# Optimization experiments

Hardware: AMD Instinct MI355X
Metric: run time of the kernel (lower is better)

Reference implementation:

```python
import jax, jax.numpy as jnp
import numpy as np

HIDDEN = 50
INPUT = 4

def setup_inputs() -> dict:
    key = jax.random.key(0)
    ks = jax.random.split(key, 7)
    B, T = 4096, 512
    s_ih = 1.0 / np.sqrt(HIDDEN)
    return {
        "x": jax.random.normal(ks[0], (B, T, INPUT), dtype=jnp.float32),
        "W_ih": jax.random.uniform(ks[1], (4 * HIDDEN, INPUT), jnp.float32, -s_ih, s_ih),
        "W_hh": jax.random.uniform(ks[2], (4 * HIDDEN, HIDDEN), jnp.float32, -s_ih, s_ih),
        "b_ih": jax.random.uniform(ks[3], (4 * HIDDEN,), jnp.float32, -s_ih, s_ih),
        "b_hh": jax.random.uniform(ks[4], (4 * HIDDEN,), jnp.float32, -s_ih, s_ih),
        "W_fc": jax.random.uniform(ks[5], (1, HIDDEN), jnp.float32, -s_ih, s_ih),
        "b_fc": jax.random.uniform(ks[6], (1,), jnp.float32, -s_ih, s_ih),
    }

def reference(x, W_ih, W_hh, b_ih, b_hh, W_fc, b_fc):
    B = x.shape[0]
    b = b_ih + b_hh  # fold biases once
    # precompute input projection for all timesteps: [B,T,4H]
    x_proj = jnp.einsum('btd,gd->btg', x, W_ih) + b
    h0 = jnp.zeros((B, HIDDEN), x.dtype)
    c0 = jnp.zeros((B, HIDDEN), x.dtype)

    def step(carry, xp_t):
        h, c = carry
        gates = xp_t + h @ W_hh.T  # [B,4H]
        i, f, g, o = jnp.split(gates, 4, axis=-1)  # PyTorch gate order i,f,g,o
        i = jax.nn.sigmoid(i)
        f = jax.nn.sigmoid(f)
        g = jnp.tanh(g)
        o = jax.nn.sigmoid(o)
        c_new = f * c + i * g
        h_new = o * jnp.tanh(c_new)
        return (h_new, c_new), None

    (h_T, _), _ = jax.lax.scan(step, (h0, c0), jnp.swapaxes(x_proj, 0, 1))
    # fc applied to last timestep only (out[:, -1, :])
    return h_T @ W_fc.T + b_fc  # [B,1]
```

## Files before the change

kernel.cpp:

```cpp
#include <hip/hip_runtime.h>


#define HID  50
#define NROW 200
#define TT   512
#define NIN  4
#define BT   16
#define KD   72
#define NW   8

typedef float f32x4 __attribute__((ext_vector_type(4)));
typedef short s16x8 __attribute__((ext_vector_type(8)));

__device__ __forceinline__ unsigned short f2bf(float f) {
    unsigned u = __builtin_bit_cast(unsigned, f);
    return (unsigned short)((u + 0x7FFF + ((u >> 16) & 1)) >> 16);
}
__device__ __forceinline__ float fast_sigmoid(float v) {
    float e = __builtin_amdgcn_exp2f(v * -1.442695040888963f);
    return __builtin_amdgcn_rcpf(1.0f + e);
}
__device__ __forceinline__ float fast_tanh(float v) {
    float e = __builtin_amdgcn_exp2f(v * -2.885390081777927f);
    return 2.0f * __builtin_amdgcn_rcpf(1.0f + e) - 1.0f;
}

__device__ __forceinline__ float wval(const float* W_hh, const float* W_ih,
                                      int rowp, int k) {
    if (rowp >= NROW) return 0.0f;
    const int ur = rowp >> 2, g = rowp & 3;
    const int a = k >> 4, b = k & 15;
    if (b <= 12) { const int u = 4 * b + a;
                   return (u < HID) ? W_hh[(g * HID + ur) * HID + u] : 0.0f; }
    if (b == 13) return W_ih[(g * HID + ur) * NIN + a];
    return 0.0f;
}

__global__ __launch_bounds__(64 * NW, 2)
void lstm_mfma3(const float* __restrict__ x,
                const float* __restrict__ W_ih,
                const float* __restrict__ W_hh,
                const float* __restrict__ b_ih,
                const float* __restrict__ b_hh,
                const float* __restrict__ W_fc,
                const float* __restrict__ b_fc,
                float* __restrict__ out)
{
    __shared__ __align__(16) unsigned short buf[2][BT][KD];
    __shared__ float red[BT];

    const int tid = threadIdx.x;
    const int w   = tid >> 6;
    const int l   = tid & 63;
    const int lr  = l & 15;
    const int lg  = l >> 4;
    const int b0  = blockIdx.x * BT;

    for (int i = tid; i < 2 * BT * KD; i += 64 * NW)
        ((unsigned short*)buf)[i] = 0;
    if (tid < BT) red[tid] = 0.0f;

    const bool two = (w < 5);
    const int  T0  = two ? w : (w + 5);
    const int  T1  = w + 5;

    s16x8 af0[2], af1[2];
    f32x4 bias0, bias1 = {0.f, 0.f, 0.f, 0.f};
    float wfc0 = 0.0f, wfc1 = 0.0f;
    {
        const int rowp = 16 * T0 + lr;
#pragma unroll
        for (int kh = 0; kh < 2; ++kh) {
            s16x8 f;
#pragma unroll
            for (int j = 0; j < 8; ++j)
                f[j] = (short)f2bf(wval(W_hh, W_ih, rowp, 32 * kh + 8 * lg + j));
            af0[kh] = f;
        }
#pragma unroll
        for (int r = 0; r < 4; ++r) {
            const int rr = 16 * T0 + 4 * lg + r;
            bias0[r] = (rr < NROW) ? (b_ih[(rr & 3) * HID + (rr >> 2)] +
                                      b_hh[(rr & 3) * HID + (rr >> 2)]) : 0.0f;
        }
        const int u = 4 * T0 + lg;
        wfc0 = (u < HID) ? W_fc[u] : 0.0f;
    }
    if (two) {
        const int rowp = 16 * T1 + lr;
#pragma unroll
        for (int kh = 0; kh < 2; ++kh) {
            s16x8 f;
#pragma unroll
            for (int j = 0; j < 8; ++j)
                f[j] = (short)f2bf(wval(W_hh, W_ih, rowp, 32 * kh + 8 * lg + j));
            af1[kh] = f;
        }
#pragma unroll
        for (int r = 0; r < 4; ++r) {
            const int rr = 16 * T1 + 4 * lg + r;
            bias1[r] = (rr < NROW) ? (b_ih[(rr & 3) * HID + (rr >> 2)] +
                                      b_hh[(rr & 3) * HID + (rr >> 2)]) : 0.0f;
        }
        const int u = 4 * T1 + lg;
        wfc1 = (u < HID) ? W_fc[u] : 0.0f;
    }

    const float* xg = x + ((size_t)(b0 + lr) * TT) * NIN + lg;
    if (w == 7) buf[0][lr][16 * lg + 13] = f2bf(xg[0]);
    __syncthreads();

    float c0 = 0.f, h0 = 0.f, c1 = 0.f, h1 = 0.f;

    for (int t = 0; t < TT; ++t) {
        const int p = t & 1;

        float xv = 0.0f;
        const bool xload = (w == 7) && (t + 1 < TT);
        if (xload) xv = xg[(size_t)(t + 1) * NIN];

        const s16x8 bf0v = *(const s16x8*)&buf[p][lr][8 * lg];
        const s16x8 bf1v = *(const s16x8*)&buf[p][lr][32 + 8 * lg];

        f32x4 a0 = bias0;
        a0 = __builtin_amdgcn_mfma_f32_16x16x32_bf16(af0[0], bf0v, a0, 0, 0, 0);
        a0 = __builtin_amdgcn_mfma_f32_16x16x32_bf16(af0[1], bf1v, a0, 0, 0, 0);
        f32x4 a1;
        if (two) {
            a1 = bias1;
            a1 = __builtin_amdgcn_mfma_f32_16x16x32_bf16(af1[0], bf0v, a1, 0, 0, 0);
            a1 = __builtin_amdgcn_mfma_f32_16x16x32_bf16(af1[1], bf1v, a1, 0, 0, 0);
        }

        if (xload) buf[p ^ 1][lr][16 * lg + 13] = f2bf(xv);

        {
            const float gi = fast_sigmoid(a0[0]);
            const float gf = fast_sigmoid(a0[1]);
            const float gg = fast_tanh(a0[2]);
            const float go = fast_sigmoid(a0[3]);
            c0 = gf * c0 + gi * gg;
            h0 = go * fast_tanh(c0);
        }
        if (two) {
            const float gi = fast_sigmoid(a1[0]);
            const float gf = fast_sigmoid(a1[1]);
            const float gg = fast_tanh(a1[2]);
            const float go = fast_sigmoid(a1[3]);
            c1 = gf * c1 + gi * gg;
            h1 = go * fast_tanh(c1);
            unsigned pk;
            asm("v_cvt_pk_bf16_f32 %0, %1, %2" : "=v"(pk) : "v"(h0), "v"(h1));
            buf[p ^ 1][lr][16 * lg + T0] = (unsigned short)pk;
            buf[p ^ 1][lr][16 * lg + T1] = (unsigned short)(pk >> 16);
        } else {
            buf[p ^ 1][lr][16 * lg + T0] = f2bf(h0);
        }
        __syncthreads();
    }

    float partial = wfc0 * h0 + wfc1 * h1;
    partial += __shfl_down(partial, 32);
    partial += __shfl_down(partial, 16);
    if (l < 16) atomicAdd(&red[l], partial);
    __syncthreads();
    if (tid < BT) out[b0 + tid] = red[tid] + b_fc[0];
}

extern "C" void kernel_launch(void* const* d_in, const int* in_sizes, int n_in,
                              void* d_out, int out_size, void* d_ws, size_t ws_size,
                              hipStream_t stream) {
    const float* x    = (const float*)d_in[0];
    const float* W_ih = (const float*)d_in[1];
    const float* W_hh = (const float*)d_in[2];
    const float* b_ih = (const float*)d_in[3];
    const float* b_hh = (const float*)d_in[4];
    const float* W_fc = (const float*)d_in[5];
    const float* b_fc = (const float*)d_in[6];
    float* out        = (float*)d_out;

    const int B = in_sizes[0] / (TT * NIN);
    lstm_mfma3<<<B / BT, 64 * NW, 0, stream>>>(x, W_ih, W_hh, b_ih, b_hh, W_fc, b_fc, out);
}
```

Measured before the change: 303.8 us.

## Preload block's x sequence into LDS as bf16 and linearize K layout

After: 326.1 us. 1.07x slower.

```diff
diff --git a/kernel.cpp b/kernel.cpp
--- a/kernel.cpp
+++ b/kernel.cpp
@@ -7,6 +7,7 @@
 #define NIN  4
 #define BT   16
 #define KD   72
+#define XSTR 17
 #define NW   8
 
 typedef float f32x4 __attribute__((ext_vector_type(4)));
@@ -26,18 +27,16 @@
 }
 
 __device__ __forceinline__ float wval(const float* W_hh, const float* W_ih,
-                                      int rowp, int k) {
+                                      int rowp, int kp) {
     if (rowp >= NROW) return 0.0f;
-    const int ur = rowp >> 2, g = rowp & 3;
-    const int a = k >> 4, b = k & 15;
-    if (b <= 12) { const int u = 4 * b + a;
-                   return (u < HID) ? W_hh[(g * HID + ur) * HID + u] : 0.0f; }
-    if (b == 13) return W_ih[(g * HID + ur) * NIN + a];
+    const int u = rowp >> 2, g = rowp & 3;
+    if (kp < HID)              return W_hh[(g * HID + u) * HID + kp];
+    if (kp >= 56 && kp < 60)   return W_ih[(g * HID + u) * NIN + (kp - 56)];
     return 0.0f;
 }
 
 __global__ __launch_bounds__(64 * NW, 2)
-void lstm_mfma3(const float* __restrict__ x,
+void lstm_mfma4(const float* __restrict__ x,
                 const float* __restrict__ W_ih,
                 const float* __restrict__ W_hh,
                 const float* __restrict__ b_ih,
@@ -47,6 +46,7 @@
                 float* __restrict__ out)
 {
     __shared__ __align__(16) unsigned short buf[2][BT][KD];
+    __shared__ uint2 xpl[TT * XSTR];
     __shared__ float red[BT];
 
     const int tid = threadIdx.x;
@@ -59,6 +59,20 @@
     for (int i = tid; i < 2 * BT * KD; i += 64 * NW)
         ((unsigned short*)buf)[i] = 0;
     if (tid < BT) red[tid] = 0.0f;
+
+    {
+        const float4* xs = (const float4*)(x + (size_t)b0 * TT * NIN);
+#pragma unroll
+        for (int it = 0; it < (TT * BT) / (64 * NW); ++it) {
+            const int e = tid + it * 64 * NW;
+            const float4 v = xs[e];
+            unsigned lo, hi;
+            asm("v_cvt_pk_bf16_f32 %0, %1, %2" : "=v"(lo) : "v"(v.x), "v"(v.y));
+            asm("v_cvt_pk_bf16_f32 %0, %1, %2" : "=v"(hi) : "v"(v.z), "v"(v.w));
+            const int brel = e >> 9, t = e & (TT - 1);
+            xpl[t * XSTR + brel] = make_uint2(lo, hi);
+        }
+    }
 
     const bool two = (w < 5);
     const int  T0  = two ? w : (w + 5);
@@ -105,9 +119,6 @@
         const int u = 4 * T1 + lg;
         wfc1 = (u < HID) ? W_fc[u] : 0.0f;
     }
-
-    const float* xg = x + ((size_t)(b0 + lr) * TT) * NIN + lg;
-    if (w == 7) buf[0][lr][16 * lg + 13] = f2bf(xg[0]);
     __syncthreads();
 
     float c0 = 0.f, h0 = 0.f, c1 = 0.f, h1 = 0.f;
@@ -115,12 +126,15 @@
     for (int t = 0; t < TT; ++t) {
         const int p = t & 1;
 
-        float xv = 0.0f;
-        const bool xload = (w == 7) && (t + 1 < TT);
-        if (xload) xv = xg[(size_t)(t + 1) * NIN];
-
         const s16x8 bf0v = *(const s16x8*)&buf[p][lr][8 * lg];
-        const s16x8 bf1v = *(const s16x8*)&buf[p][lr][32 + 8 * lg];
+        s16x8 bf1v;
+        if (lg == 3) {
+            const uint2 xv = xpl[t * XSTR + lr];
+            const uint4 tmp = {xv.x, xv.y, 0u, 0u};
+            bf1v = __builtin_bit_cast(s16x8, tmp);
+        } else {
+            bf1v = *(const s16x8*)&buf[p][lr][32 + 8 * lg];
+        }
 
         f32x4 a0 = bias0;
         a0 = __builtin_amdgcn_mfma_f32_16x16x32_bf16(af0[0], bf0v, a0, 0, 0, 0);
@@ -132,8 +146,6 @@
             a1 = __builtin_amdgcn_mfma_f32_16x16x32_bf16(af1[1], bf1v, a1, 0, 0, 0);
         }
 
-        if (xload) buf[p ^ 1][lr][16 * lg + 13] = f2bf(xv);
-
         {
             const float gi = fast_sigmoid(a0[0]);
             const float gf = fast_sigmoid(a0[1]);
@@ -141,6 +153,7 @@
             const float go = fast_sigmoid(a0[3]);
             c0 = gf * c0 + gi * gg;
             h0 = go * fast_tanh(c0);
+            buf[p ^ 1][lr][4 * T0 + lg] = f2bf(h0);
         }
         if (two) {
             const float gi = fast_sigmoid(a1[0]);
@@ -149,12 +162,7 @@
             const float go = fast_sigmoid(a1[3]);
             c1 = gf * c1 + gi * gg;
             h1 = go * fast_tanh(c1);
-            unsigned pk;
-            asm("v_cvt_pk_bf16_f32 %0, %1, %2" : "=v"(pk) : "v"(h0), "v"(h1));
-            buf[p ^ 1][lr][16 * lg + T0] = (unsigned short)pk;
-            buf[p ^ 1][lr][16 * lg + T1] = (unsigned short)(pk >> 16);
-        } else {
-            buf[p ^ 1][lr][16 * lg + T0] = f2bf(h0);
+            buf[p ^ 1][lr][4 * T1 + lg] = f2bf(h1);
         }
         __syncthreads();
     }
@@ -180,5 +188,5 @@
     float* out        = (float*)d_out;
 
     const int B = in_sizes[0] / (TT * NIN);
-    lstm_mfma3<<<B / BT, 64 * NW, 0, stream>>>(x, W_ih, W_hh, b_ih, b_hh, W_fc, b_fc, out);
+    lstm_mfma4<<<B / BT, 64 * NW, 0, stream>>>(x, W_ih, W_hh, b_ih, b_hh, W_fc, b_fc, out);
 }
```

## Interleave four independent batch tiles per block to overlap recurrent step latency

Applied to the files above, without the earlier changes.

Result: slower. 850.5 us (+180.0%).

```diff
diff --git a/kernel.cpp b/kernel.cpp
--- a/kernel.cpp
+++ b/kernel.cpp
@@ -8,6 +8,7 @@
 #define BT   16
 #define KD   72
 #define NW   8
+#define G    4
 
 typedef float f32x4 __attribute__((ext_vector_type(4)));
 typedef short s16x8 __attribute__((ext_vector_type(8)));
@@ -26,18 +27,16 @@
 }
 
 __device__ __forceinline__ float wval(const float* W_hh, const float* W_ih,
-                                      int rowp, int k) {
+                                      int rowp, int kp) {
     if (rowp >= NROW) return 0.0f;
-    const int ur = rowp >> 2, g = rowp & 3;
-    const int a = k >> 4, b = k & 15;
-    if (b <= 12) { const int u = 4 * b + a;
-                   return (u < HID) ? W_hh[(g * HID + ur) * HID + u] : 0.0f; }
-    if (b == 13) return W_ih[(g * HID + ur) * NIN + a];
+    const int u = rowp >> 2, g = rowp & 3;
+    if (kp < HID) return W_hh[(g * HID + u) * HID + kp];
+    if (kp >= 56 && !(kp & 1)) return W_ih[(g * HID + u) * NIN + ((kp - 56) >> 1)];
     return 0.0f;
 }
 
-__global__ __launch_bounds__(64 * NW, 2)
-void lstm_mfma3(const float* __restrict__ x,
+__global__ __launch_bounds__(64 * NW, 1)
+void lstm_mfma7(const float* __restrict__ x,
                 const float* __restrict__ W_ih,
                 const float* __restrict__ W_hh,
                 const float* __restrict__ b_ih,
@@ -46,19 +45,19 @@
                 const float* __restrict__ b_fc,
                 float* __restrict__ out)
 {
-    __shared__ __align__(16) unsigned short buf[2][BT][KD];
-    __shared__ float red[BT];
+    __shared__ __align__(16) unsigned short buf[G][2][BT][KD];
+    __shared__ float red[G * BT];
 
     const int tid = threadIdx.x;
     const int w   = tid >> 6;
     const int l   = tid & 63;
     const int lr  = l & 15;
     const int lg  = l >> 4;
-    const int b0  = blockIdx.x * BT;
+    const int b0  = blockIdx.x * (BT * G);
 
-    for (int i = tid; i < 2 * BT * KD; i += 64 * NW)
+    for (int i = tid; i < G * 2 * BT * KD; i += 64 * NW)
         ((unsigned short*)buf)[i] = 0;
-    if (tid < BT) red[tid] = 0.0f;
+    if (tid < G * BT) red[tid] = 0.0f;
 
     const bool two = (w < 5);
     const int  T0  = two ? w : (w + 5);
@@ -105,66 +104,73 @@
         const int u = 4 * T1 + lg;
         wfc1 = (u < HID) ? W_fc[u] : 0.0f;
     }
-
-    const float* xg = x + ((size_t)(b0 + lr) * TT) * NIN + lg;
-    if (w == 7) buf[0][lr][16 * lg + 13] = f2bf(xg[0]);
     __syncthreads();
 
-    float c0 = 0.f, h0 = 0.f, c1 = 0.f, h1 = 0.f;
+    const int gx = w & 3;
+    const float* xgp = x + ((size_t)(b0 + 16 * gx + lr) * TT) * NIN + lg;
+    if (w >= 4)
+        buf[gx][0][lr][56 + 2 * lg] = f2bf(xgp[0]);
+    __syncthreads();
+
+    float c0[G], h0[G], c1[G], h1[G];
+#pragma unroll
+    for (int g = 0; g < G; ++g) { c0[g] = h0[g] = c1[g] = h1[g] = 0.f; }
 
     for (int t = 0; t < TT; ++t) {
         const int p = t & 1;
 
         float xv = 0.0f;
-        const bool xload = (w == 7) && (t + 1 < TT);
-        if (xload) xv = xg[(size_t)(t + 1) * NIN];
+        const bool xduty = (w >= 4) && (t + 1 < TT);
+        if (xduty) xv = xgp[(size_t)(t + 1) * NIN];
 
-        const s16x8 bf0v = *(const s16x8*)&buf[p][lr][8 * lg];
-        const s16x8 bf1v = *(const s16x8*)&buf[p][lr][32 + 8 * lg];
+#pragma unroll
+        for (int g = 0; g < G; ++g) {
+            const s16x8 bf0v = *(const s16x8*)&buf[g][p][lr][8 * lg];
+            const s16x8 bf1v = *(const s16x8*)&buf[g][p][lr][32 + 8 * lg];
 
-        f32x4 a0 = bias0;
-        a0 = __builtin_amdgcn_mfma_f32_16x16x32_bf16(af0[0], bf0v, a0, 0, 0, 0);
-        a0 = __builtin_amdgcn_mfma_f32_16x16x32_bf16(af0[1], bf1v, a0, 0, 0, 0);
-        f32x4 a1;
-        if (two) {
-            a1 = bias1;
-            a1 = __builtin_amdgcn_mfma_f32_16x16x32_bf16(af1[0], bf0v, a1, 0, 0, 0);
-            a1 = __builtin_amdgcn_mfma_f32_16x16x32_bf16(af1[1], bf1v, a1, 0, 0, 0);
+            f32x4 a0 = __builtin_amdgcn_mfma_f32_16x16x32_bf16(af0[0], bf0v, bias0, 0, 0, 0);
+            a0       = __builtin_amdgcn_mfma_f32_16x16x32_bf16(af0[1], bf1v, a0,    0, 0, 0);
+            f32x4 a1;
+            if (two) {
+                a1 = __builtin_amdgcn_mfma_f32_16x16x32_bf16(af1[0], bf0v, bias1, 0, 0, 0);
+                a1 = __builtin_amdgcn_mfma_f32_16x16x32_bf16(af1[1], bf1v, a1,    0, 0, 0);
+            }
+
+            {
+                const float gi = fast_sigmoid(a0[0]);
+                const float gf = fast_sigmoid(a0[1]);
+                const float gg = fast_tanh(a0[2]);
+                const float go = fast_sigmoid(a0[3]);
+                c0[g] = gf * c0[g] + gi * gg;
+                h0[g] = go * fast_tanh(c0[g]);
+                buf[g][p ^ 1][lr][4 * T0 + lg] = f2bf(h0[g]);
+            }
+            if (two) {
+                const float gi = fast_sigmoid(a1[0]);
+                const float gf = fast_sigmoid(a1[1]);
+                const float gg = fast_tanh(a1[2]);
+                const float go = fast_sigmoid(a1[3]);
+                c1[g] = gf * c1[g] + gi * gg;
+                h1[g] = go * fast_tanh(c1[g]);
+                buf[g][p ^ 1][lr][4 * T1 + lg] = f2bf(h1[g]);
+            }
         }
 
-        if (xload) buf[p ^ 1][lr][16 * lg + 13] = f2bf(xv);
+        if (xduty)
+            buf[gx][p ^ 1][lr][56 + 2 * lg] = f2bf(xv);
 
-        {
-            const float gi = fast_sigmoid(a0[0]);
-            const float gf = fast_sigmoid(a0[1]);
-            const float gg = fast_tanh(a0[2]);
-            const float go = fast_sigmoid(a0[3]);
-            c0 = gf * c0 + gi * gg;
-            h0 = go * fast_tanh(c0);
-        }
-        if (two) {
-            const float gi = fast_sigmoid(a1[0]);
-            const float gf = fast_sigmoid(a1[1]);
-            const float gg = fast_tanh(a1[2]);
-            const float go = fast_sigmoid(a1[3]);
-            c1 = gf * c1 + gi * gg;
-            h1 = go * fast_tanh(c1);
-            unsigned pk;
-            asm("v_cvt_pk_bf16_f32 %0, %1, %2" : "=v"(pk) : "v"(h0), "v"(h1));
-            buf[p ^ 1][lr][16 * lg + T0] = (unsigned short)pk;
-            buf[p ^ 1][lr][16 * lg + T1] = (unsigned short)(pk >> 16);
-        } else {
-            buf[p ^ 1][lr][16 * lg + T0] = f2bf(h0);
-        }
         __syncthreads();
     }
 
-    float partial = wfc0 * h0 + wfc1 * h1;
-    partial += __shfl_down(partial, 32);
-    partial += __shfl_down(partial, 16);
-    if (l < 16) atomicAdd(&red[l], partial);
+#pragma unroll
+    for (int g = 0; g < G; ++g) {
+        float partial = wfc0 * h0[g] + wfc1 * h1[g];
+        partial += __shfl_down(partial, 32);
+        partial += __shfl_down(partial, 16);
+        if (l < BT) atomicAdd(&red[g * BT + l], partial);
+    }
     __syncthreads();
-    if (tid < BT) out[b0 + tid] = red[tid] + b_fc[0];
+    if (tid < G * BT) out[b0 + tid] = red[tid] + b_fc[0];
 }
 
 extern "C" void kernel_launch(void* const* d_in, const int* in_sizes, int n_in,
@@ -180,5 +186,6 @@
     float* out        = (float*)d_out;
 
     const int B = in_sizes[0] / (TT * NIN);
-    lstm_mfma3<<<B / BT, 64 * NW, 0, stream>>>(x, W_ih, W_hh, b_ih, b_hh, W_fc, b_fc, out);
+    lstm_mfma7<<<B / (BT * G), 64 * NW, 0, stream>>>(x, W_ih, W_hh, b_ih, b_hh,
+                                                     W_fc, b_fc, out);
 }
```
